# Kernel tuning notes

Hardware: AMD Instinct MI355X
Metric: run time of the kernel (lower is better)

The kernel has to match this reference:

```python
import jax, jax.numpy as jnp
import numpy as np


def setup_inputs() -> dict:
    key = jax.random.key(0)
    k1, k2, k3 = jax.random.split(key, 3)
    b, n, d, K = 8, 16384, 128, 128
    X = jax.random.normal(k1, (b, n, d), dtype=jnp.float32)
    C = jax.random.normal(k2, (K, d), dtype=jnp.float32)
    # module init: scale.data.uniform_(-1, 0)
    S = -jax.random.uniform(k3, (K,), dtype=jnp.float32)
    return {"X": X, "C": C, "S": S}


def reference(X, C, S):
    """Soft VQ encoding: scaled L2 -> softmax assignment -> residual aggregation.

    X: (b, n, d) features; C: (k, d) codewords; S: (k,) scales.
    Returns E: (b, k, d) aggregated residuals, same math as
    aggregate(softmax(scaled_l2(X, C, S), dim=2), X, C).
    """
    X2 = jnp.sum(X * X, axis=-1, keepdims=True)          # (b, n, 1)
    C2 = jnp.sum(C * C, axis=-1)                          # (k,)
    XC = jnp.einsum('bnd,kd->bnk', X, C)                  # (b, n, k)
    D = S * (X2 + C2 - 2.0 * XC)                          # scaled L2, (b, n, k)
    A = jax.nn.softmax(D, axis=-1)                        # assignment weights
    # E[b,k,:] = sum_n A[b,n,k] * (X[b,n,:] - C[k,:])
    #          = (A^T X)[b,k,:] - (sum_n A[b,n,k]) * C[k,:]
    E = jnp.einsum('bnk,bnd->bkd', A, X) - jnp.sum(A, axis=1)[..., None] * C[None]
    return E
```

## Files before the change

kernel.cpp:

```cpp
#include <hip/hip_runtime.h>


#define NN   16384
#define ND   128
#define NK   128
#define NC   64
#define TT   4
#define BPB  64
#define CBP  136
#define XTP  72
#define ATP  72

typedef __bf16 bf16x8 __attribute__((ext_vector_type(8)));
typedef float  f32x4  __attribute__((ext_vector_type(4)));

union CU  { __bf16 b[8]; unsigned short u[8]; bf16x8 v; };
union HH4 { __bf16 b[4]; ushort4 s; };

__device__ __forceinline__ float bf2f(unsigned short u) {
    return __uint_as_float(((unsigned int)u) << 16);
}

__global__ __launch_bounds__(256, 2) void vq_main(
    const float* __restrict__ Xg, const float* __restrict__ Cg,
    const float* __restrict__ Sg, unsigned short* __restrict__ Pg)
{
    __shared__ __align__(16) unsigned short sCb[NK * CBP];
    __shared__ __align__(16) unsigned short sXT[ND * XTP];
    __shared__ __align__(16) unsigned short sAt[NK * ATP];
    __shared__ __align__(16) float2 sST[NK];
    __shared__ __align__(16) float  sC2[NK];

    const int tid  = threadIdx.x;
    const int lane = tid & 63;
    const int wave = tid >> 6;
    const int l15  = lane & 15;
    const int quad = lane >> 4;
    const int bid  = blockIdx.x;
    const int b    = bid >> 6;
    const int bg   = bid & (BPB - 1);

    #pragma unroll
    for (int it = 0; it < 16; ++it) {
        int flat = it * 256 + tid;
        int row  = flat >> 5;
        int c4   = flat & 31;
        float4 v = reinterpret_cast<const float4*>(Cg)[row * 32 + c4];
        HH4 h;
        h.b[0] = (__bf16)v.x; h.b[1] = (__bf16)v.y;
        h.b[2] = (__bf16)v.z; h.b[3] = (__bf16)v.w;
        *reinterpret_cast<ushort4*>(&sCb[row * CBP + c4 * 4]) = h.s;
        float ss = v.x*v.x + v.y*v.y + v.z*v.z + v.w*v.w;
        ss += __shfl_xor(ss, 1);
        ss += __shfl_xor(ss, 2);
        ss += __shfl_xor(ss, 4);
        ss += __shfl_xor(ss, 8);
        ss += __shfl_xor(ss, 16);
        if ((lane & 31) == 0) sC2[row] = ss;
    }
    __syncthreads();
    if (tid < NK) {
        float s = Sg[tid];
        sST[tid] = make_float2(s, s * sC2[tid]);
    }

    f32x4 eacc[2][8];
    #pragma unroll
    for (int i = 0; i < 2; ++i)
        #pragma unroll
        for (int j = 0; j < 8; ++j)
            eacc[i][j] = (f32x4){0.f, 0.f, 0.f, 0.f};
    f32x4 cntacc[2];
    cntacc[0] = (f32x4){0.f, 0.f, 0.f, 0.f};
    cntacc[1] = (f32x4){0.f, 0.f, 0.f, 0.f};

    CU one8;
    #pragma unroll
    for (int j = 0; j < 8; ++j) one8.u[j] = 0x3F80;

    const float* Xb = Xg + (size_t)b * (NN * ND);
    const int rloc = wave * 16 + l15;

    float4 raw[4];
    {
        const float* rp0 = Xb + (size_t)(bg * TT * NC + rloc) * ND;
        raw[0] = *reinterpret_cast<const float4*>(rp0 + quad * 8);
        raw[1] = *reinterpret_cast<const float4*>(rp0 + quad * 8 + 4);
        raw[2] = *reinterpret_cast<const float4*>(rp0 + 32 + quad * 8);
        raw[3] = *reinterpret_cast<const float4*>(rp0 + 32 + quad * 8 + 4);
    }

    #pragma unroll 1
    for (int t = 0; t < TT; ++t) {
        const int chunk = bg * TT + t;
        const float* rp = Xb + (size_t)(chunk * NC + rloc) * ND;

        float4 va2 = *reinterpret_cast<const float4*>(rp + 64 + quad * 8);
        float4 vb2 = *reinterpret_cast<const float4*>(rp + 64 + quad * 8 + 4);
        float4 va3 = *reinterpret_cast<const float4*>(rp + 96 + quad * 8);
        float4 vb3 = *reinterpret_cast<const float4*>(rp + 96 + quad * 8 + 4);

        CU cu[4];
        float x2 = 0.f;
        #pragma unroll
        for (int ks = 0; ks < 2; ++ks) {
            float4 va = raw[ks * 2], vb = raw[ks * 2 + 1];
            x2 += va.x*va.x + va.y*va.y + va.z*va.z + va.w*va.w;
            x2 += vb.x*vb.x + vb.y*vb.y + vb.z*vb.z + vb.w*vb.w;
            cu[ks].b[0] = (__bf16)va.x; cu[ks].b[1] = (__bf16)va.y;
            cu[ks].b[2] = (__bf16)va.z; cu[ks].b[3] = (__bf16)va.w;
            cu[ks].b[4] = (__bf16)vb.x; cu[ks].b[5] = (__bf16)vb.y;
            cu[ks].b[6] = (__bf16)vb.z; cu[ks].b[7] = (__bf16)vb.w;
        }
        {
            x2 += va2.x*va2.x + va2.y*va2.y + va2.z*va2.z + va2.w*va2.w;
            x2 += vb2.x*vb2.x + vb2.y*vb2.y + vb2.z*vb2.z + vb2.w*vb2.w;
            cu[2].b[0] = (__bf16)va2.x; cu[2].b[1] = (__bf16)va2.y;
            cu[2].b[2] = (__bf16)va2.z; cu[2].b[3] = (__bf16)va2.w;
            cu[2].b[4] = (__bf16)vb2.x; cu[2].b[5] = (__bf16)vb2.y;
            cu[2].b[6] = (__bf16)vb2.z; cu[2].b[7] = (__bf16)vb2.w;
            x2 += va3.x*va3.x + va3.y*va3.y + va3.z*va3.z + va3.w*va3.w;
            x2 += vb3.x*vb3.x + vb3.y*vb3.y + vb3.z*vb3.z + vb3.w*vb3.w;
            cu[3].b[0] = (__bf16)va3.x; cu[3].b[1] = (__bf16)va3.y;
            cu[3].b[2] = (__bf16)va3.z; cu[3].b[3] = (__bf16)va3.w;
            cu[3].b[4] = (__bf16)vb3.x; cu[3].b[5] = (__bf16)vb3.y;
            cu[3].b[6] = (__bf16)vb3.z; cu[3].b[7] = (__bf16)vb3.w;
        }
        x2 += __shfl_xor(x2, 16);
        x2 += __shfl_xor(x2, 32);

        __syncthreads();

        if (t + 1 < TT) {
            const float* rpn = rp + (size_t)NC * ND;
            raw[0] = *reinterpret_cast<const float4*>(rpn + quad * 8);
            raw[1] = *reinterpret_cast<const float4*>(rpn + quad * 8 + 4);
            raw[2] = *reinterpret_cast<const float4*>(rpn + 32 + quad * 8);
            raw[3] = *reinterpret_cast<const float4*>(rpn + 32 + quad * 8 + 4);
        }

        #pragma unroll
        for (int ks = 0; ks < 4; ++ks) {
            #pragma unroll
            for (int j = 0; j < 8; ++j) {
                int d  = ks * 32 + quad * 8 + j;
                int rs = rloc ^ (((d >> 3) & 3) << 3);
                sXT[d * XTP + rs] = cu[ks].u[j];
            }
        }

        f32x4 dacc[8];
        #pragma unroll
        for (int mt = 0; mt < 8; ++mt) {
            f32x4 acc = (f32x4){0.f, 0.f, 0.f, 0.f};
            #pragma unroll
            for (int ks = 0; ks < 4; ++ks) {
                bf16x8 af = *reinterpret_cast<const bf16x8*>(
                    &sCb[(mt * 16 + l15) * CBP + ks * 32 + quad * 8]);
                acc = __builtin_amdgcn_mfma_f32_16x16x32_bf16(af, cu[ks].v, acc, 0, 0, 0);
            }
            dacc[mt] = acc;
        }

        float mx = -3.0e38f;
        #pragma unroll
        for (int mt = 0; mt < 8; ++mt) {
            float4 s01 = *reinterpret_cast<const float4*>(&sST[mt * 16 + quad * 4]);
            float4 s23 = *reinterpret_cast<const float4*>(&sST[mt * 16 + quad * 4 + 2]);
            float dv0 = s01.x * fmaf(-2.f, dacc[mt][0], x2) + s01.y;
            float dv1 = s01.z * fmaf(-2.f, dacc[mt][1], x2) + s01.w;
            float dv2 = s23.x * fmaf(-2.f, dacc[mt][2], x2) + s23.y;
            float dv3 = s23.z * fmaf(-2.f, dacc[mt][3], x2) + s23.w;
            dacc[mt][0] = dv0; dacc[mt][1] = dv1;
            dacc[mt][2] = dv2; dacc[mt][3] = dv3;
            mx = fmaxf(mx, fmaxf(fmaxf(dv0, dv1), fmaxf(dv2, dv3)));
        }
        mx = fmaxf(mx, __shfl_xor(mx, 16));
        mx = fmaxf(mx, __shfl_xor(mx, 32));
        float ls = 0.f;
        #pragma unroll
        for (int mt = 0; mt < 8; ++mt) {
            #pragma unroll
            for (int r = 0; r < 4; ++r) {
                float e = __expf(dacc[mt][r] - mx);
                dacc[mt][r] = e;
                ls += e;
            }
        }
        ls += __shfl_xor(ls, 16);
        ls += __shfl_xor(ls, 32);
        const float inv = 1.0f / ls;

        #pragma unroll
        for (int mt = 0; mt < 8; ++mt) {
            #pragma unroll
            for (int r = 0; r < 4; ++r) {
                float a = dacc[mt][r] * inv;
                *reinterpret_cast<__bf16*>(
                    &sAt[(mt * 16 + quad * 4 + r) * ATP + rloc]) = (__bf16)a;
            }
        }

        __syncthreads();

        #pragma unroll
        for (int mt2 = 0; mt2 < 2; ++mt2) {
            const int cwrow = wave * 32 + mt2 * 16 + l15;
            bf16x8 a0 = *reinterpret_cast<const bf16x8*>(&sAt[cwrow * ATP + quad * 8]);
            bf16x8 a1 = *reinterpret_cast<const bf16x8*>(&sAt[cwrow * ATP + 32 + quad * 8]);
            cntacc[mt2] = __builtin_amdgcn_mfma_f32_16x16x32_bf16(a0, one8.v, cntacc[mt2], 0, 0, 0);
            cntacc[mt2] = __builtin_amdgcn_mfma_f32_16x16x32_bf16(a1, one8.v, cntacc[mt2], 0, 0, 0);
            #pragma unroll
            for (int dt = 0; dt < 8; ++dt) {
                const int drow = dt * 16 + l15;
                const int sw = ((drow >> 3) & 3) << 3;
                const unsigned short* xp = &sXT[drow * XTP];
                bf16x8 b0 = *reinterpret_cast<const bf16x8*>(&xp[(quad * 8) ^ sw]);
                bf16x8 b1 = *reinterpret_cast<const bf16x8*>(&xp[(32 + quad * 8) ^ sw]);
                eacc[mt2][dt] = __builtin_amdgcn_mfma_f32_16x16x32_bf16(a0, b0, eacc[mt2][dt], 0, 0, 0);
                eacc[mt2][dt] = __builtin_amdgcn_mfma_f32_16x16x32_bf16(a1, b1, eacc[mt2][dt], 0, 0, 0);
            }
        }
    }

    unsigned short* P = Pg + (size_t)bid * (NK * ND);
    #pragma unroll
    for (int mt2 = 0; mt2 < 2; ++mt2) {
        #pragma unroll
        for (int r = 0; r < 4; ++r) {
            const int cw = wave * 32 + mt2 * 16 + quad * 4 + r;
            const float cc = cntacc[mt2][r];
            const float* crow = Cg + cw * ND;
            #pragma unroll
            for (int dt = 0; dt < 8; ++dt) {
                const int d = dt * 16 + l15;
                *reinterpret_cast<__bf16*>(&P[cw * ND + d]) =
                    (__bf16)(eacc[mt2][dt][r] - cc * crow[d]);
            }
        }
    }
}

__global__ __launch_bounds__(256) void vq_reduce(
    const unsigned short* __restrict__ Pg, float* __restrict__ Eg)
{
    const int g  = blockIdx.x * 256 + threadIdx.x;
    const int b  = g >> 12;
    const int i4 = g & 4095;
    const unsigned short* base = Pg + (size_t)(b * BPB) * (NK * ND) + i4 * 4;
    float a0 = 0.f, a1 = 0.f, a2 = 0.f, a3 = 0.f;
    #pragma unroll 8
    for (int j = 0; j < BPB; ++j) {
        ushort4 v = *reinterpret_cast<const ushort4*>(base + (size_t)j * (NK * ND));
        a0 += bf2f(v.x); a1 += bf2f(v.y); a2 += bf2f(v.z); a3 += bf2f(v.w);
    }
    float4 o; o.x = a0; o.y = a1; o.z = a2; o.w = a3;
    *reinterpret_cast<float4*>(Eg + (size_t)b * (NK * ND) + i4 * 4) = o;
}

extern "C" void kernel_launch(void* const* d_in, const int* in_sizes, int n_in,
                              void* d_out, int out_size, void* d_ws, size_t ws_size,
                              hipStream_t stream) {
    const float* X = (const float*)d_in[0];
    const float* C = (const float*)d_in[1];
    const float* S = (const float*)d_in[2];
    float* E = (float*)d_out;
    (void)n_in; (void)in_sizes; (void)out_size; (void)ws_size;

    unsigned short* P = (unsigned short*)d_ws;

    hipLaunchKernelGGL(vq_main,   dim3(512), dim3(256), 0, stream, X, C, S, P);
    hipLaunchKernelGGL(vq_reduce, dim3(128), dim3(256), 0, stream, P, E);
}
```

Before: 115.4 us.

## XOR-swizzle unpadded LDS tiles, cache half of codebook in registers, drop softmax max

Replaces the padded transposed LDS layouts for X and assignment tiles with 64-wide rows using an 8-group XOR swizzle, which cuts LDS footprint and avoids bank conflicts without padding. Half of the codebook MFMA operands are held in registers across iterations, so fewer LDS reads are needed per chunk. The softmax max-subtraction pass and its cross-lane reductions are removed. This relies on the scaled distances (non-positive scale times non-negative distance) never overflowing exp, and it can underflow when every logit is very negative. The extra register-resident operands raise VGPR pressure at the 2-block occupancy target.

```diff
diff --git a/kernel.cpp b/kernel.cpp
--- a/kernel.cpp
+++ b/kernel.cpp
@@ -8,8 +8,6 @@
 #define TT   4
 #define BPB  64
 #define CBP  136
-#define XTP  72
-#define ATP  72
 
 typedef __bf16 bf16x8 __attribute__((ext_vector_type(8)));
 typedef float  f32x4  __attribute__((ext_vector_type(4)));
@@ -26,8 +24,8 @@
     const float* __restrict__ Sg, unsigned short* __restrict__ Pg)
 {
     __shared__ __align__(16) unsigned short sCb[NK * CBP];
-    __shared__ __align__(16) unsigned short sXT[ND * XTP];
-    __shared__ __align__(16) unsigned short sAt[NK * ATP];
+    __shared__ __align__(16) unsigned short sXT[ND * 64];
+    __shared__ __align__(16) unsigned short sAt[NK * 64];
     __shared__ __align__(16) float2 sST[NK];
     __shared__ __align__(16) float  sC2[NK];
 
@@ -64,6 +62,14 @@
         sST[tid] = make_float2(s, s * sC2[tid]);
     }
 
+    bf16x8 chs[8][2];
+    #pragma unroll
+    for (int mt = 0; mt < 8; ++mt)
+        #pragma unroll
+        for (int ks = 0; ks < 2; ++ks)
+            chs[mt][ks] = *reinterpret_cast<const bf16x8*>(
+                &sCb[(mt * 16 + l15) * CBP + ks * 32 + quad * 8]);
+
     f32x4 eacc[2][8];
     #pragma unroll
     for (int i = 0; i < 2; ++i)
@@ -80,6 +86,8 @@
 
     const float* Xb = Xg + (size_t)b * (NN * ND);
     const int rloc = wave * 16 + l15;
+    const int rg   = rloc >> 3;
+    const int rlow = rloc & 7;
 
     float4 raw[4];
     {
@@ -141,11 +149,11 @@
 
         #pragma unroll
         for (int ks = 0; ks < 4; ++ks) {
+            const int gx = (rg ^ (ks * 4 + quad)) & 7;
             #pragma unroll
             for (int j = 0; j < 8; ++j) {
-                int d  = ks * 32 + quad * 8 + j;
-                int rs = rloc ^ (((d >> 3) & 3) << 3);
-                sXT[d * XTP + rs] = cu[ks].u[j];
+                int d = ks * 32 + quad * 8 + j;
+                sXT[d * 64 + gx * 8 + rlow] = cu[ks].u[j];
             }
         }
 
@@ -153,8 +161,10 @@
         #pragma unroll
         for (int mt = 0; mt < 8; ++mt) {
             f32x4 acc = (f32x4){0.f, 0.f, 0.f, 0.f};
-            #pragma unroll
-            for (int ks = 0; ks < 4; ++ks) {
+            acc = __builtin_amdgcn_mfma_f32_16x16x32_bf16(chs[mt][0], cu[0].v, acc, 0, 0, 0);
+            acc = __builtin_amdgcn_mfma_f32_16x16x32_bf16(chs[mt][1], cu[1].v, acc, 0, 0, 0);
+            #pragma unroll
+            for (int ks = 2; ks < 4; ++ks) {
                 bf16x8 af = *reinterpret_cast<const bf16x8*>(
                     &sCb[(mt * 16 + l15) * CBP + ks * 32 + quad * 8]);
                 acc = __builtin_amdgcn_mfma_f32_16x16x32_bf16(af, cu[ks].v, acc, 0, 0, 0);
@@ -162,30 +172,18 @@
             dacc[mt] = acc;
         }
 
-        float mx = -3.0e38f;
+        float ls = 0.f;
         #pragma unroll
         for (int mt = 0; mt < 8; ++mt) {
             float4 s01 = *reinterpret_cast<const float4*>(&sST[mt * 16 + quad * 4]);
             float4 s23 = *reinterpret_cast<const float4*>(&sST[mt * 16 + quad * 4 + 2]);
-            float dv0 = s01.x * fmaf(-2.f, dacc[mt][0], x2) + s01.y;
-            float dv1 = s01.z * fmaf(-2.f, dacc[mt][1], x2) + s01.w;
-            float dv2 = s23.x * fmaf(-2.f, dacc[mt][2], x2) + s23.y;
-            float dv3 = s23.z * fmaf(-2.f, dacc[mt][3], x2) + s23.w;
-            dacc[mt][0] = dv0; dacc[mt][1] = dv1;
-            dacc[mt][2] = dv2; dacc[mt][3] = dv3;
-            mx = fmaxf(mx, fmaxf(fmaxf(dv0, dv1), fmaxf(dv2, dv3)));
-        }
-        mx = fmaxf(mx, __shfl_xor(mx, 16));
-        mx = fmaxf(mx, __shfl_xor(mx, 32));
-        float ls = 0.f;
-        #pragma unroll
-        for (int mt = 0; mt < 8; ++mt) {
-            #pragma unroll
-            for (int r = 0; r < 4; ++r) {
-                float e = __expf(dacc[mt][r] - mx);
-                dacc[mt][r] = e;
-                ls += e;
-            }
+            float e0 = __expf(s01.x * fmaf(-2.f, dacc[mt][0], x2) + s01.y);
+            float e1 = __expf(s01.z * fmaf(-2.f, dacc[mt][1], x2) + s01.w);
+            float e2 = __expf(s23.x * fmaf(-2.f, dacc[mt][2], x2) + s23.y);
+            float e3 = __expf(s23.z * fmaf(-2.f, dacc[mt][3], x2) + s23.w);
+            dacc[mt][0] = e0; dacc[mt][1] = e1;
+            dacc[mt][2] = e2; dacc[mt][3] = e3;
+            ls += (e0 + e1) + (e2 + e3);
         }
         ls += __shfl_xor(ls, 16);
         ls += __shfl_xor(ls, 32);
@@ -196,8 +194,10 @@
             #pragma unroll
             for (int r = 0; r < 4; ++r) {
                 float a = dacc[mt][r] * inv;
+                const int cw = mt * 16 + quad * 4 + r;
+                const int gx = (rg ^ (cw >> 3)) & 7;
                 *reinterpret_cast<__bf16*>(
-                    &sAt[(mt * 16 + quad * 4 + r) * ATP + rloc]) = (__bf16)a;
+                    &sAt[cw * 64 + gx * 8 + rlow]) = (__bf16)a;
             }
         }
 
@@ -206,17 +206,22 @@
         #pragma unroll
         for (int mt2 = 0; mt2 < 2; ++mt2) {
             const int cwrow = wave * 32 + mt2 * 16 + l15;
-            bf16x8 a0 = *reinterpret_cast<const bf16x8*>(&sAt[cwrow * ATP + quad * 8]);
-            bf16x8 a1 = *reinterpret_cast<const bf16x8*>(&sAt[cwrow * ATP + 32 + quad * 8]);
+            const int cx = (cwrow >> 3) & 7;
+            bf16x8 a0 = *reinterpret_cast<const bf16x8*>(
+                &sAt[cwrow * 64 + ((quad ^ cx) & 7) * 8]);
+            bf16x8 a1 = *reinterpret_cast<const bf16x8*>(
+                &sAt[cwrow * 64 + (((4 + quad) ^ cx) & 7) * 8]);
             cntacc[mt2] = __builtin_amdgcn_mfma_f32_16x16x32_bf16(a0, one8.v, cntacc[mt2], 0, 0, 0);
             cntacc[mt2] = __builtin_amdgcn_mfma_f32_16x16x32_bf16(a1, one8.v, cntacc[mt2], 0, 0, 0);
             #pragma unroll
             for (int dt = 0; dt < 8; ++dt) {
                 const int drow = dt * 16 + l15;
-                const int sw = ((drow >> 3) & 3) << 3;
-                const unsigned short* xp = &sXT[drow * XTP];
-                bf16x8 b0 = *reinterpret_cast<const bf16x8*>(&xp[(quad * 8) ^ sw]);
-                bf16x8 b1 = *reinterpret_cast<const bf16x8*>(&xp[(32 + quad * 8) ^ sw]);
+                const int dx = (drow >> 3) & 7;
+                const unsigned short* xp = &sXT[drow * 64];
+                bf16x8 b0 = *reinterpret_cast<const bf16x8*>(
+                    &xp[((quad ^ dx) & 7) * 8]);
+                bf16x8 b1 = *reinterpret_cast<const bf16x8*>(
+                    &xp[(((4 + quad) ^ dx) & 7) * 8]);
                 eacc[mt2][dt] = __builtin_amdgcn_mfma_f32_16x16x32_bf16(a0, b0, eacc[mt2][dt], 0, 0, 0);
                 eacc[mt2][dt] = __builtin_amdgcn_mfma_f32_16x16x32_bf16(a1, b1, eacc[mt2][dt], 0, 0, 0);
             }
```

Result: slower. 128.1 us (+11.0%).
